# Kernel optimization log

Hardware: AMD Instinct MI355X
Metric: run time of the kernel (lower is better)

## Reference

```python
import jax, jax.numpy as jnp
import numpy as np

B, S, E, H, DK = 2, 1024, 1024, 128, 8  # batch, seq, embed_dim, num_heads, d_k (= n_wires)


def setup_inputs() -> dict:
    key = jax.random.key(0)
    ks = jax.random.split(key, 10)
    sc = 1.0 / np.sqrt(E)
    inp = {
        "x": jax.random.normal(ks[0], (B, S, E), dtype=jnp.float32),
        "Wq": jax.random.normal(ks[1], (E, E), dtype=jnp.float32) * sc,
        "bq": jnp.zeros((E,), jnp.float32),
        "Wk": jax.random.normal(ks[2], (E, E), dtype=jnp.float32) * sc,
        "bk": jnp.zeros((E,), jnp.float32),
        "Wv": jax.random.normal(ks[3], (E, E), dtype=jnp.float32) * sc,
        "bv": jnp.zeros((E,), jnp.float32),
        "phi": jax.random.uniform(ks[4], (H, DK), jnp.float32, -np.pi, np.pi),  # trainable RX angles per head
        "Wo": jax.random.normal(ks[5], (E, E), dtype=jnp.float32) * sc,
        "bo": jnp.zeros((E,), jnp.float32),
    }
    return inp


def reference(x, Wq, bq, Wk, bk, Wv, bv, phi, Wo, bo):
    b, s, e = x.shape
    h, dk = phi.shape
    # QKV projections (k, v are computed but unused in the original forward)
    q = (x @ Wq.T + bq).reshape(b, s, h, dk).transpose(0, 2, 1, 3)  # [B,H,S,DK]
    k = (x @ Wk.T + bk).reshape(b, s, h, dk).transpose(0, 2, 1, 3)
    v = (x @ Wv.T + bv).reshape(b, s, h, dk).transpose(0, 2, 1, 3)
    del k, v  # dead in original math
    # Quantum circuit per head: RX(q_i) then RX(phi_i) on |0>, measure PauliZ.
    # RX angles on same wire add; <Z> after RX(theta)|0> = cos(theta).
    out = jnp.cos(q + phi[None, :, None, :])  # [B,H,S,DK]
    scores = jnp.einsum("bhsd,bhtd->bhst", out, out) / np.sqrt(dk)
    attn = jax.nn.softmax(scores, axis=-1)  # dropout is identity in eval mode
    ctx = jnp.einsum("bhst,bhtd->bhsd", attn, out)
    ctx = ctx.transpose(0, 2, 1, 3).reshape(b, s, e)
    return ctx @ Wo.T + bo
```

## Files before the change

### kernel.cpp

```cpp
#include <hip/hip_runtime.h>
#include <hip/hip_bf16.h>

#define Bv  2
#define Sv  1024
#define Ev  1024
#define Hv  128
#define DKv 8
#define Mv  (Bv*Sv)

typedef __attribute__((ext_vector_type(8))) short short8;
typedef __attribute__((ext_vector_type(4))) float f32x4;

static __device__ __forceinline__ short f2b(float f) {
    __hip_bfloat16 h = __float2bfloat16(f);
    return *reinterpret_cast<short*>(&h);
}

static __device__ __forceinline__ unsigned cvtpk(float a, float b) {
    unsigned r;
    asm("v_cvt_pk_bf16_f32 %0, %1, %2" : "=v"(r) : "v"(a), "v"(b));
    return r;
}

static __device__ __forceinline__ float hexp2(float x) {
    return __builtin_amdgcn_exp2f(x);
}

static __device__ __forceinline__ void gload16(const void* g, void* l) {
    __builtin_amdgcn_global_load_lds(
        (const __attribute__((address_space(1))) unsigned int*)g,
        (__attribute__((address_space(3))) unsigned int*)l, 16, 0, 0);
}

__global__ __launch_bounds__(256)
void cvt_all(const float* __restrict__ x, const float* __restrict__ wq,
             const float* __restrict__ wo, short* __restrict__ xb,
             short* __restrict__ wqb, short* __restrict__ wob)
{
    const int b = blockIdx.x;
    const float* src; short* dst; int i;
    if (b < 1024)      { src = x;  dst = xb;  i = b * 256 + threadIdx.x; }
    else if (b < 1536) { src = wq; dst = wqb; i = (b - 1024) * 256 + threadIdx.x; }
    else               { src = wo; dst = wob; i = (b - 1536) * 256 + threadIdx.x; }
    float4 a = ((const float4*)src)[2 * i];
    float4 c = ((const float4*)src)[2 * i + 1];
    uint4 o;
    o.x = cvtpk(a.x, a.y); o.y = cvtpk(a.z, a.w);
    o.z = cvtpk(c.x, c.y); o.w = cvtpk(c.z, c.w);
    ((uint4*)dst)[i] = o;
}

template<int EPI>
__global__ __launch_bounds__(256)
void gemm_bf16(const short* __restrict__ A, const short* __restrict__ W,
               const float* __restrict__ bias, const float* __restrict__ phi,
               void* __restrict__ outv)
{
    __shared__ short As[2][64 * 64];
    __shared__ short Bs[2][64 * 64];

    const int t    = threadIdx.x;
    const int w    = t >> 6, lane = t & 63;
    const int c    = lane & 15, g = lane >> 4;
    const int cs   = c & 7;
    const int wr   = w >> 1,  wc = w & 1;
    const int tm   = blockIdx.y * 64, tn = blockIdx.x * 64;
    const int lr   = lane >> 3;
    const int lcs  = ((lane & 7) ^ lr) * 8;

    f32x4 acc[2][2] = {};

    #define STAGE(s, k0)                                                        \
        _Pragma("unroll")                                                       \
        for (int j = 0; j < 2; j++) {                                           \
            const int row = w * 16 + j * 8;                                     \
            gload16(&A[(size_t)(tm + row + lr) * Ev + (k0) + lcs], &As[s][row * 64]); \
            gload16(&W[(size_t)(tn + row + lr) * Ev + (k0) + lcs], &Bs[s][row * 64]); \
        }

    STAGE(0, 0)
    __syncthreads();

    for (int ks = 0; ks < 16; ks++) {
        const int cur = ks & 1;
        if (ks < 15) { STAGE(cur ^ 1, (ks + 1) * 64) }
        #pragma unroll
        for (int kk = 0; kk < 64; kk += 32) {
            const int s0 = ((kk >> 3) + g) ^ cs;
            short8 af[2], bf[2];
            #pragma unroll
            for (int m = 0; m < 2; m++)
                af[m] = *(const short8*)&As[cur][(wr * 32 + m * 16 + c) * 64 + s0 * 8];
            #pragma unroll
            for (int n = 0; n < 2; n++)
                bf[n] = *(const short8*)&Bs[cur][(wc * 32 + n * 16 + c) * 64 + s0 * 8];
            #pragma unroll
            for (int m = 0; m < 2; m++)
                #pragma unroll
                for (int n = 0; n < 2; n++)
                    acc[m][n] = __builtin_amdgcn_mfma_f32_16x16x32_bf16(af[m], bf[n], acc[m][n], 0, 0, 0);
        }
        __syncthreads();
    }

    #pragma unroll
    for (int i = 0; i < 2; i++) {
        #pragma unroll
        for (int j = 0; j < 2; j++) {
            const int n = tn + wc * 32 + j * 16 + c;
            #pragma unroll
            for (int r = 0; r < 4; r++) {
                const int m = tm + wr * 32 + i * 16 + 4 * g + r;
                const float v = acc[i][j][r];
                if (EPI == 0) {
                    float q = __cosf(v + bias[n] + phi[n]);
                    const int bb = m >> 10, ss = m & (Sv - 1);
                    const int hh = n >> 3,  dd = n & (DKv - 1);
                    ((short*)outv)[(((size_t)bb * Hv + hh) * Sv + ss) * DKv + dd] = f2b(q);
                } else {
                    ((float*)outv)[(size_t)m * Ev + n] = v + bias[n];
                }
            }
        }
    }
    #undef STAGE
}

__global__ __launch_bounds__(256)
void attn_mfma(const short* __restrict__ om, short* __restrict__ ctx)
{
    __shared__ short K_lds[Sv * DKv];
    __shared__ short Vt[DKv * 1032];
    __shared__ short P_lds[4][16][40];

    const int t  = threadIdx.x;
    const int bh = blockIdx.x;
    const short* base = om + (size_t)bh * (Sv * DKv);

    #pragma unroll
    for (int r = 0; r < 4; r++) {
        const int k = r * 256 + t;
        int4 row = ((const int4*)base)[k];
        ((int4*)K_lds)[k] = row;
        union { int4 v; short s[8]; } u; u.v = row;
        #pragma unroll
        for (int d = 0; d < 8; d++) Vt[d * 1032 + k] = u.s[d];
    }
    __syncthreads();

    const int w = t >> 6, lane = t & 63;
    const int c = lane & 15, g = lane >> 4;
    const int q0 = blockIdx.y * 64 + w * 16;

    short8 qf = {};
    if (g == 0) qf = *(const short8*)&K_lds[(q0 + c) * 8];

    f32x4 ctx_acc = {0.f, 0.f, 0.f, 0.f};
    float lsum = 0.f;

    for (int kt = 0; kt < Sv; kt += 32) {
        short8 kf0 = {}, kf1 = {};
        if (g == 0) {
            kf0 = *(const short8*)&K_lds[(kt +      c) * 8];
            kf1 = *(const short8*)&K_lds[(kt + 16 + c) * 8];
        }
        const f32x4 z = {0.f, 0.f, 0.f, 0.f};
        f32x4 s0 = __builtin_amdgcn_mfma_f32_16x16x32_bf16(kf0, qf, z, 0, 0, 0);
        f32x4 s1 = __builtin_amdgcn_mfma_f32_16x16x32_bf16(kf1, qf, z, 0, 0, 0);

        float p[8];
        #pragma unroll
        for (int r = 0; r < 4; r++) {
            p[r]     = hexp2(s0[r] * 0.5100697f);
            p[4 + r] = hexp2(s1[r] * 0.5100697f);
        }
        lsum += ((p[0] + p[1]) + (p[2] + p[3])) + ((p[4] + p[5]) + (p[6] + p[7]));

        uint2 w0, w1;
        w0.x = cvtpk(p[0], p[1]); w0.y = cvtpk(p[2], p[3]);
        w1.x = cvtpk(p[4], p[5]); w1.y = cvtpk(p[6], p[7]);
        *(uint2*)&P_lds[w][c][4 * g]      = w0;
        *(uint2*)&P_lds[w][c][16 + 4 * g] = w1;

        short8 pf = *(const short8*)&P_lds[w][c][8 * g];
        short8 vf = {};
        if (c < 8) vf = *(const short8*)&Vt[c * 1032 + kt + 8 * g];
        ctx_acc = __builtin_amdgcn_mfma_f32_16x16x32_bf16(pf, vf, ctx_acc, 0, 0, 0);
    }

    lsum += __shfl_xor(lsum, 16);
    lsum += __shfl_xor(lsum, 32);
    float L[4];
    #pragma unroll
    for (int r = 0; r < 4; r++) L[r] = __shfl(lsum, 4 * g + r);

    if (c < 8) {
        const int b = bh >> 7, h = bh & (Hv - 1);
        #pragma unroll
        for (int r = 0; r < 4; r++) {
            const int q = q0 + 4 * g + r;
            ctx[((size_t)(b * Sv + q)) * Ev + h * DKv + c] = f2b(ctx_acc[r] / L[r]);
        }
    }
}

extern "C" void kernel_launch(void* const* d_in, const int* in_sizes, int n_in,
                              void* d_out, int out_size, void* d_ws, size_t ws_size,
                              hipStream_t stream)
{
    const float* x   = (const float*)d_in[0];
    const float* Wq  = (const float*)d_in[1];
    const float* bq  = (const float*)d_in[2];
    const float* phi = (const float*)d_in[7];
    const float* Wo  = (const float*)d_in[8];
    const float* bo  = (const float*)d_in[9];
    float* out = (float*)d_out;

    char* ws = (char*)d_ws;
    short* xb  = (short*)ws;
    short* ctx = xb;
    short* om  = (short*)(ws + (4 << 20));
    short* Wqb = (short*)(ws + (8 << 20));
    short* Wob = (short*)(ws + (10 << 20));

    cvt_all<<<dim3(2048), 256, 0, stream>>>(x, Wq, Wo, xb, Wqb, Wob);

    const dim3 gg(Ev / 64, Mv / 64);
    gemm_bf16<0><<<gg, 256, 0, stream>>>(xb, Wqb, bq, phi, (void*)om);
    attn_mfma<<<dim3(Bv * Hv, Sv / 64), 256, 0, stream>>>(om, ctx);
    gemm_bf16<1><<<gg, 256, 0, stream>>>(ctx, Wob, bo, nullptr, (void*)out);
}
```

Baseline: 174.1 us.

## Fold softmax scale into Q, compute row sums via MFMA, swizzle GEMM blocks

```diff
diff --git a/kernel.cpp b/kernel.cpp
--- a/kernel.cpp
+++ b/kernel.cpp
@@ -8,6 +8,9 @@
 #define DKv 8
 #define Mv  (Bv*Sv)
 
+#define SQC  0.7141916f
+#define ISQC 1.4001855f
+
 typedef __attribute__((ext_vector_type(8))) short short8;
 typedef __attribute__((ext_vector_type(4))) float f32x4;
 
@@ -38,15 +41,15 @@
              short* __restrict__ wqb, short* __restrict__ wob)
 {
     const int b = blockIdx.x;
-    const float* src; short* dst; int i;
+    const float* src; short* dst; int i; float sc = 1.0f;
     if (b < 1024)      { src = x;  dst = xb;  i = b * 256 + threadIdx.x; }
     else if (b < 1536) { src = wq; dst = wqb; i = (b - 1024) * 256 + threadIdx.x; }
-    else               { src = wo; dst = wob; i = (b - 1536) * 256 + threadIdx.x; }
+    else               { src = wo; dst = wob; i = (b - 1536) * 256 + threadIdx.x; sc = ISQC; }
     float4 a = ((const float4*)src)[2 * i];
     float4 c = ((const float4*)src)[2 * i + 1];
     uint4 o;
-    o.x = cvtpk(a.x, a.y); o.y = cvtpk(a.z, a.w);
-    o.z = cvtpk(c.x, c.y); o.w = cvtpk(c.z, c.w);
+    o.x = cvtpk(a.x * sc, a.y * sc); o.y = cvtpk(a.z * sc, a.w * sc);
+    o.z = cvtpk(c.x * sc, c.y * sc); o.w = cvtpk(c.z * sc, c.w * sc);
     ((uint4*)dst)[i] = o;
 }
 
@@ -64,7 +67,9 @@
     const int c    = lane & 15, g = lane >> 4;
     const int cs   = c & 7;
     const int wr   = w >> 1,  wc = w & 1;
-    const int tm   = blockIdx.y * 64, tn = blockIdx.x * 64;
+    const int bid  = blockIdx.x;
+    const int swz  = (bid & 7) * 64 + (bid >> 3);
+    const int tn   = (swz & 15) * 64, tm = (swz >> 4) * 64;
     const int lr   = lane >> 3;
     const int lcs  = ((lane & 7) ^ lr) * 8;
 
@@ -113,7 +118,7 @@
                 const int m = tm + wr * 32 + i * 16 + 4 * g + r;
                 const float v = acc[i][j][r];
                 if (EPI == 0) {
-                    float q = __cosf(v + bias[n] + phi[n]);
+                    float q = __cosf(v + bias[n] + phi[n]) * SQC;
                     const int bb = m >> 10, ss = m & (Sv - 1);
                     const int hh = n >> 3,  dd = n & (DKv - 1);
                     ((short*)outv)[(((size_t)bb * Hv + hh) * Sv + ss) * DKv + dd] = f2b(q);
@@ -127,15 +132,20 @@
 }
 
 __global__ __launch_bounds__(256)
-void attn_mfma(const short* __restrict__ om, short* __restrict__ ctx)
+void attn_mfma(const short* __restrict__ om, short* __restrict__ ctx, int qbase)
 {
     __shared__ short K_lds[Sv * DKv];
     __shared__ short Vt[DKv * 1032];
     __shared__ short P_lds[4][16][40];
+    __shared__ __align__(16) short zpage[8];
+    __shared__ __align__(16) short opage[8];
 
     const int t  = threadIdx.x;
     const int bh = blockIdx.x;
     const short* base = om + (size_t)bh * (Sv * DKv);
+
+    if (t < 8) zpage[t] = 0;
+    else if (t < 16) opage[t - 8] = 0x3F80;
 
     #pragma unroll
     for (int r = 0; r < 4; r++) {
@@ -150,56 +160,49 @@
 
     const int w = t >> 6, lane = t & 63;
     const int c = lane & 15, g = lane >> 4;
-    const int q0 = blockIdx.y * 64 + w * 16;
+    const int q0 = qbase + blockIdx.y * 64 + w * 16;
 
     short8 qf = {};
     if (g == 0) qf = *(const short8*)&K_lds[(q0 + c) * 8];
 
-    f32x4 ctx_acc = {0.f, 0.f, 0.f, 0.f};
-    float lsum = 0.f;
+    const short* kp0 = (g == 0) ? &K_lds[c * 8]        : zpage;
+    const short* kp1 = (g == 0) ? &K_lds[(16 + c) * 8] : zpage;
+    const int   kadv = (g == 0) ? 32 * 8 : 0;
+    const short* vp  = (c < 8) ? &Vt[c * 1032 + 8 * g] : (c == 8 ? opage : zpage);
+    const int   vadv = (c < 8) ? 32 : 0;
+
+    f32x4 acc = {0.f, 0.f, 0.f, 0.f};
+    const f32x4 z = {0.f, 0.f, 0.f, 0.f};
 
     for (int kt = 0; kt < Sv; kt += 32) {
-        short8 kf0 = {}, kf1 = {};
-        if (g == 0) {
-            kf0 = *(const short8*)&K_lds[(kt +      c) * 8];
-            kf1 = *(const short8*)&K_lds[(kt + 16 + c) * 8];
-        }
-        const f32x4 z = {0.f, 0.f, 0.f, 0.f};
+        short8 kf0 = *(const short8*)kp0;  kp0 += kadv;
+        short8 kf1 = *(const short8*)kp1;  kp1 += kadv;
         f32x4 s0 = __builtin_amdgcn_mfma_f32_16x16x32_bf16(kf0, qf, z, 0, 0, 0);
         f32x4 s1 = __builtin_amdgcn_mfma_f32_16x16x32_bf16(kf1, qf, z, 0, 0, 0);
 
-        float p[8];
-        #pragma unroll
-        for (int r = 0; r < 4; r++) {
-            p[r]     = hexp2(s0[r] * 0.5100697f);
-            p[4 + r] = hexp2(s1[r] * 0.5100697f);
-        }
-        lsum += ((p[0] + p[1]) + (p[2] + p[3])) + ((p[4] + p[5]) + (p[6] + p[7]));
-
         uint2 w0, w1;
-        w0.x = cvtpk(p[0], p[1]); w0.y = cvtpk(p[2], p[3]);
-        w1.x = cvtpk(p[4], p[5]); w1.y = cvtpk(p[6], p[7]);
+        w0.x = cvtpk(hexp2(s0[0]), hexp2(s0[1]));
+        w0.y = cvtpk(hexp2(s0[2]), hexp2(s0[3]));
+        w1.x = cvtpk(hexp2(s1[0]), hexp2(s1[1]));
+        w1.y = cvtpk(hexp2(s1[2]), hexp2(s1[3]));
         *(uint2*)&P_lds[w][c][4 * g]      = w0;
         *(uint2*)&P_lds[w][c][16 + 4 * g] = w1;
 
         short8 pf = *(const short8*)&P_lds[w][c][8 * g];
-        short8 vf = {};
-        if (c < 8) vf = *(const short8*)&Vt[c * 1032 + kt + 8 * g];
-        ctx_acc = __builtin_amdgcn_mfma_f32_16x16x32_bf16(pf, vf, ctx_acc, 0, 0, 0);
-    }
-
-    lsum += __shfl_xor(lsum, 16);
-    lsum += __shfl_xor(lsum, 32);
+        short8 vf = *(const short8*)vp;  vp += vadv;
+        acc = __builtin_amdgcn_mfma_f32_16x16x32_bf16(pf, vf, acc, 0, 0, 0);
+    }
+
     float L[4];
     #pragma unroll
-    for (int r = 0; r < 4; r++) L[r] = __shfl(lsum, 4 * g + r);
+    for (int r = 0; r < 4; r++) L[r] = __shfl(acc[r], (lane & 48) | 8);
 
     if (c < 8) {
         const int b = bh >> 7, h = bh & (Hv - 1);
         #pragma unroll
         for (int r = 0; r < 4; r++) {
             const int q = q0 + 4 * g + r;
-            ctx[((size_t)(b * Sv + q)) * Ev + h * DKv + c] = f2b(ctx_acc[r] / L[r]);
+            ctx[((size_t)(b * Sv + q)) * Ev + h * DKv + c] = f2b(acc[r] / L[r]);
         }
     }
 }
@@ -225,8 +228,8 @@
 
     cvt_all<<<dim3(2048), 256, 0, stream>>>(x, Wq, Wo, xb, Wqb, Wob);
 
-    const dim3 gg(Ev / 64, Mv / 64);
-    gemm_bf16<0><<<gg, 256, 0, stream>>>(xb, Wqb, bq, phi, (void*)om);
-    attn_mfma<<<dim3(Bv * Hv, Sv / 64), 256, 0, stream>>>(om, ctx);
-    gemm_bf16<1><<<gg, 256, 0, stream>>>(ctx, Wob, bo, nullptr, (void*)out);
-}
+    gemm_bf16<0><<<dim3(512), 256, 0, stream>>>(xb, Wqb, bq, phi, (void*)om);
+    attn_mfma<<<dim3(Bv * Hv, 8), 256, 0, stream>>>(om, ctx, 0);
+    attn_mfma<<<dim3(Bv * Hv, 8), 256, 0, stream>>>(om, ctx, 512);
+    gemm_bf16<1><<<dim3(512), 256, 0, stream>>>(ctx, Wob, bo, nullptr, (void*)out);
+}
```

Measured after the change: 168.3 us. 1.03x faster.
